# Kernel tuning notes

Measured on AMD Instinct MI355X. Metric: run time of the kernel, lower is better.

Reference implementation:

```python
import jax, jax.numpy as jnp
import numpy as np

B, S = 4096, 4096
NS, FDIM = 16, 64


def _ln(x, g, b):
    mu = jnp.mean(x, axis=-1, keepdims=True)
    v = jnp.mean((x - mu) ** 2, axis=-1, keepdims=True)
    return (x - mu) / jnp.sqrt(v + 1e-5) * g + b


def _rolling_vol_mean(returns, w):
    # mean over all length-w windows of unbiased std (matches per-window torch.std loop)
    Bn, L = returns.shape
    z = jnp.zeros((Bn, 1), returns.dtype)
    c1 = jnp.concatenate([z, jnp.cumsum(returns, axis=1)], axis=1)
    c2 = jnp.concatenate([z, jnp.cumsum(returns * returns, axis=1)], axis=1)
    s = c1[:, w:] - c1[:, :-w]    # [B, L-w+1] window sums
    s2 = c2[:, w:] - c2[:, :-w]
    var = (s2 - s * s / w) / (w - 1)
    return jnp.mean(jnp.sqrt(jnp.maximum(var, 0.0)), axis=1, keepdims=True)


def setup_inputs() -> dict:
    key = jax.random.key(0)
    ks = jax.random.split(key, 24)
    r = lambda i, shp: jax.random.normal(ks[i], shp, jnp.float32) * 0.05
    return {
        'price_series': jax.random.uniform(ks[0], (B, S, 1), jnp.float32) * 10.0 + 1.0,
        're_W': r(1, (4, 4, 64)), 're_b': r(2, (4, 64)),
        're_g': jnp.ones((4, 64), jnp.float32), 're_beta': jnp.zeros((4, 64), jnp.float32),
        'rh_W1': r(3, (256, 64)), 'rh_b1': r(4, (64,)), 'rh_W2': r(5, (64, 4)), 'rh_b2': r(6, (4,)),
        'rv_W': r(7, (3, 128)), 'rv_b': r(8, (128,)),
        'rv_g': jnp.ones((128,), jnp.float32), 'rv_beta': jnp.zeros((128,), jnp.float32),
        'vs_W': r(9, (128, 128)), 'vs_b': r(10, (128,)),
        'vs_g': jnp.ones((128,), jnp.float32), 'vs_beta': jnp.zeros((128,), jnp.float32),
        'vc_W1': r(11, (256, 64)), 'vc_b1': r(12, (64,)), 'vc_W2': r(13, (64, 4)), 'vc_b2': r(14, (4,)),
        'emb': r(15, (NS, FDIM)),
        'cn_W1': r(16, (576, 128)), 'cn_b1': r(17, (128,)),
        'cn_W2': r(18, (128, 64)), 'cn_b2': r(19, (64,)),
        'cn_W3': r(20, (64, 1)), 'cn_b3': r(21, (1,)),
    }


def reference(price_series, re_W, re_b, re_g, re_beta, rh_W1, rh_b1, rh_W2, rh_b2,
              rv_W, rv_b, rv_g, rv_beta, vs_W, vs_b, vs_g, vs_beta,
              vc_W1, vc_b1, vc_W2, vc_b2, emb, cn_W1, cn_b1, cn_W2, cn_b2, cn_W3, cn_b3):
    prices = price_series[:, :, 0]            # [B,S]
    Bn, Sn = prices.shape
    # --- MarketRegimeEncoder: SMA-20 via prefix sums (the per-step torch loop) ---
    cs = jnp.cumsum(prices, axis=1)
    shifted = jnp.concatenate([jnp.zeros((Bn, 20), prices.dtype), cs[:, :-20]], axis=1)
    counts = jnp.minimum(jnp.arange(Sn) + 1, 20).astype(prices.dtype)
    sma20 = (cs - shifted) / counts           # (sma_5 is computed but unused in original)
    trend = jnp.mean((prices - sma20) / (sma20 + 1e-8), axis=1, keepdims=True)
    p10 = prices[:, Sn - 10:Sn - 9]
    momentum = (prices[:, -1:] - p10) / (p10 + 1e-8)
    pmean = jnp.mean(prices, axis=1, keepdims=True)
    mean_rev = (prices[:, -1:] - pmean) / (pmean + 1e-8)
    pstd = jnp.std(prices, axis=1, keepdims=True, ddof=1)
    cycle = pstd / (pmean + 1e-8)
    combined = jnp.concatenate([trend, momentum, mean_rev, cycle], axis=1)  # [B,4]
    h = jax.nn.relu(jnp.einsum('bi,kio->bko', combined, re_W) + re_b[None])  # [B,4,64]
    h = _ln(h, re_g[None], re_beta[None])
    regime_features = h.reshape(Bn, -1)        # [B,256] (trend|momentum|mean_rev|cycle)
    logits = jax.nn.relu(regime_features @ rh_W1 + rh_b1) @ rh_W2 + rh_b2
    regime_probs = jax.nn.softmax(logits, axis=1)
    # --- VolatilityEncodingModule ---
    logp = jnp.log(jnp.maximum(price_series, 1e-8))
    returns = jnp.diff(logp, axis=1)[:, :, 0]  # [B,S-1]
    vol_in = jnp.concatenate([_rolling_vol_mean(returns, w) for w in (5, 10, 20)], axis=1)  # [B,3]
    rv = _ln(jax.nn.relu(vol_in @ rv_W + rv_b), rv_g, rv_beta)
    vs = _ln(jax.nn.relu(rv @ vs_W + vs_b), vs_g, vs_beta)
    vol_features = jnp.concatenate([rv, vs], axis=1)  # [B,256]
    vlogits = jax.nn.relu(vol_features @ vc_W1 + vc_b1) @ vc_W2 + vc_b2
    vol_regime = jax.nn.softmax(vlogits, axis=1)
    # --- OptionsStrategyEncoder: vectorized over strategies ---
    mv = jnp.concatenate([regime_features, vol_features], axis=1)  # [B,512]
    mvp = mv @ cn_W1[:512]                    # [B,128]
    ep = emb @ cn_W1[512:]                    # [NS,128]
    h1 = jax.nn.relu(mvp[:, None, :] + ep[None, :, :] + cn_b1)  # [B,NS,128]
    h2 = jax.nn.relu(h1 @ cn_W2 + cn_b2)      # [B,NS,64]
    scores = (h2 @ cn_W3 + cn_b3)[:, :, 0]    # [B,NS]
    return regime_features, regime_probs, vol_features, vol_regime, scores
```

## Files before the change

### kernel.cpp

```cpp
#include <hip/hip_runtime.h>
#include <math.h>

#define NROWS 4096
#define SLEN  4096
#define RETN  4095
#define STRD  274

__global__ __launch_bounds__(256) void k_ep(const float* __restrict__ emb,
                                            const float* __restrict__ cn_W1,
                                            const float* __restrict__ cn_b1,
                                            float* __restrict__ ep) {
    int idx = blockIdx.x * 256 + threadIdx.x;
    if (idx >= 16 * 128) return;
    int n = idx >> 7, o = idx & 127;
    float acc = cn_b1[o];
    const float* w = cn_W1 + 512 * 128;
    for (int i = 0; i < 64; ++i) acc = fmaf(emb[n * 64 + i], w[i * 128 + o], acc);
    ep[idx] = acc;
}

__global__ __launch_bounds__(256, 4) void k_stats(const float* __restrict__ price,
                                                  float* __restrict__ combined,
                                                  float* __restrict__ volin) {
    __shared__ float scm[16 * STRD];
    __shared__ float red[6][4];

    const int tid = threadIdx.x;
    const int row = blockIdx.x;
    const float* pr = price + (size_t)row * SLEN;

    float pA = 0.f, pB = 0.f;
    if (tid == 0) { pA = pr[SLEN - 10]; pB = pr[SLEN - 1]; }

    if (tid < 32) scm[(tid & 15) * STRD + (tid >> 4)] = 0.f;
    scm[(tid & 15) * STRD + 258 + (tid >> 4)] = 0.f;

    #pragma unroll
    for (int it = 0; it < 4; ++it) {
        const int i = it * 256 + tid;
        const float4 v = ((const float4*)pr)[i];
        const int base = (4 * (i & 3)) * STRD + (i >> 2) + 2;
        scm[base]            = v.x;
        scm[base + STRD]     = v.y;
        scm[base + 2 * STRD] = v.z;
        scm[base + 3 * STRD] = v.w;
    }
    __syncthreads();

    const int s0 = tid * 16;

    float hb[20];
    #pragma unroll
    for (int k = 0; k < 20; ++k)
        hb[k] = (k < 4) ? scm[(12 + k) * STRD + tid]
                        : scm[(k - 4) * STRD + (tid + 1)];
    float x_[16];
    #pragma unroll
    for (int d = 0; d < 16; ++d) x_[d] = scm[d * STRD + (tid + 2)];

    float W = 0.f;
    #pragma unroll
    for (int k = 0; k < 20; ++k) W += hb[k];
    float st = 0.f, s1p = 0.f, s2p = 0.f;
    #pragma unroll
    for (int d = 0; d < 16; ++d) {
        const float x = x_[d];
        W += x - hb[d];
        float inv_cnt = 0.05f;
        if (s0 == 0)                 inv_cnt = 1.0f / (float)(d + 1);
        else if (s0 == 16 && d < 3)  inv_cnt = 1.0f / (float)(17 + d);
        const float sma = W * inv_cnt;
        st  = fmaf(x - sma, __builtin_amdgcn_rcpf(sma + 1e-8f), st);
        s1p += x;
        s2p = fmaf(x, x, s2p);
    }

    float lg[17];
    #pragma unroll
    for (int d = 0; d < 16; ++d) lg[d] = __builtin_amdgcn_logf(fmaxf(x_[d], 1e-8f));
    lg[16] = __builtin_amdgcn_logf(fmaxf(scm[0 * STRD + (tid + 3)], 1e-8f));
    float rs[20];
    #pragma unroll
    for (int d = 0; d < 16; ++d) rs[d] = lg[d + 1] - lg[d];

    __syncthreads();

    #pragma unroll
    for (int d = 0; d < 16; ++d)
        if (s0 + d < RETN) scm[d * STRD + (tid + 2)] = rs[d];
    __syncthreads();

    #pragma unroll
    for (int j = 0; j < 4; ++j) rs[16 + j] = scm[j * STRD + (tid + 3)];

    float S5 = 0.f, Q5 = 0.f, S10 = 0.f, Q10 = 0.f, S20 = 0.f, Q20 = 0.f;
    #pragma unroll
    for (int j = 0; j < 20; ++j) {
        const float x = rs[j];
        S20 += x; Q20 = fmaf(x, x, Q20);
        if (j < 10) { S10 += x; Q10 = fmaf(x, x, Q10); }
        if (j < 5)  { S5  += x; Q5  = fmaf(x, x, Q5); }
    }

    #define SQT(S, Q, invw, invw1) \
        __builtin_amdgcn_sqrtf(fmaxf(fmaf(-(S) * (invw), (S), (Q)) * (invw1), 0.f))
    #define X5(d)  ((d) < 15 ? rs[(d) + 5]  : scm[4 * STRD + (tid + 3)])
    #define X10(d) ((d) < 10 ? rs[(d) + 10] : scm[((d) - 6) * STRD + (tid + 3)])
    #define X20(d) ((d) < 12 ? scm[((d) + 4) * STRD + (tid + 3)] \
                             : scm[((d) - 12) * STRD + (tid + 4)])

    float v5 = 0.f, v10 = 0.f, v20 = 0.f;
    if (tid < 254) {
        #pragma unroll
        for (int d = 0; d < 16; ++d) {
            v5  += SQT(S5,  Q5,  0.2f,  0.25f);
            v10 += SQT(S10, Q10, 0.1f,  1.f / 9.f);
            v20 += SQT(S20, Q20, 0.05f, 1.f / 19.f);
            const float xo = rs[d], qo = xo * xo;
            const float a5 = X5(d), a10 = X10(d), a20 = X20(d);
            S5  += a5  - xo;  Q5  = fmaf(a5,  a5,  Q5)  - qo;
            S10 += a10 - xo;  Q10 = fmaf(a10, a10, Q10) - qo;
            S20 += a20 - xo;  Q20 = fmaf(a20, a20, Q20) - qo;
        }
    } else {
        #pragma unroll
        for (int d = 0; d < 16; ++d) {
            const int i = s0 + d;
            if (i < 4091) v5  += SQT(S5,  Q5,  0.2f,  0.25f);
            if (i < 4086) v10 += SQT(S10, Q10, 0.1f,  1.f / 9.f);
            if (i < 4076) v20 += SQT(S20, Q20, 0.05f, 1.f / 19.f);
            const float xo = rs[d], qo = xo * xo;
            const float a5 = X5(d), a10 = X10(d), a20 = X20(d);
            S5  += a5  - xo;  Q5  = fmaf(a5,  a5,  Q5)  - qo;
            S10 += a10 - xo;  Q10 = fmaf(a10, a10, Q10) - qo;
            S20 += a20 - xo;  Q20 = fmaf(a20, a20, Q20) - qo;
        }
    }
    #undef SQT
    #undef X5
    #undef X10
    #undef X20

    {
        float vals[6] = {s1p, s2p, st, v5, v10, v20};
        const int lane = tid & 63, wid = tid >> 6;
        #pragma unroll
        for (int v = 0; v < 6; ++v) {
            float x = vals[v];
            for (int o = 32; o > 0; o >>= 1) x += __shfl_xor(x, o, 64);
            if (lane == 0) red[v][wid] = x;
        }
    }
    __syncthreads();
    if (tid == 0) {
        const float sum_p  = red[0][0] + red[0][1] + red[0][2] + red[0][3];
        const float sum_p2 = red[1][0] + red[1][1] + red[1][2] + red[1][3];
        const float sum_t  = red[2][0] + red[2][1] + red[2][2] + red[2][3];
        const float sv5    = red[3][0] + red[3][1] + red[3][2] + red[3][3];
        const float sv10   = red[4][0] + red[4][1] + red[4][2] + red[4][3];
        const float sv20   = red[5][0] + red[5][1] + red[5][2] + red[5][3];
        const float pmean = sum_p * (1.f / 4096.f);
        const float varp  = fmaf(-sum_p * (1.f / 4096.f), sum_p, sum_p2) * (1.f / 4095.f);
        const float pstd  = __builtin_amdgcn_sqrtf(fmaxf(varp, 0.f));
        const float ipm   = __builtin_amdgcn_rcpf(pmean + 1e-8f);
        combined[row * 4 + 0] = sum_t * (1.f / 4096.f);
        combined[row * 4 + 1] = (pB - pA) * __builtin_amdgcn_rcpf(pA + 1e-8f);
        combined[row * 4 + 2] = (pB - pmean) * ipm;
        combined[row * 4 + 3] = pstd * ipm;
        const float LN2 = 0.6931471805599453f;
        volin[row * 3 + 0] = sv5  * (LN2 / 4091.f);
        volin[row * 3 + 1] = sv10 * (LN2 / 4086.f);
        volin[row * 3 + 2] = sv20 * (LN2 / 4076.f);
    }
}

__global__ __launch_bounds__(256) void k_mlp(const float* __restrict__ combined,
                                             const float* __restrict__ volin,
                                             const float* __restrict__ re_W,  const float* __restrict__ re_b,
                                             const float* __restrict__ re_g,  const float* __restrict__ re_be,
                                             const float* __restrict__ rh_W1, const float* __restrict__ rh_b1,
                                             const float* __restrict__ rh_W2, const float* __restrict__ rh_b2,
                                             const float* __restrict__ rv_W,  const float* __restrict__ rv_b,
                                             const float* __restrict__ rv_g,  const float* __restrict__ rv_be,
                                             const float* __restrict__ vs_W,  const float* __restrict__ vs_b,
                                             const float* __restrict__ vs_g,  const float* __restrict__ vs_be,
                                             const float* __restrict__ vc_W1, const float* __restrict__ vc_b1,
                                             const float* __restrict__ vc_W2, const float* __restrict__ vc_b2,
                                             float* __restrict__ out_rf, float* __restrict__ out_rp,
                                             float* __restrict__ out_vf, float* __restrict__ out_vr) {
    __shared__ float rf_lds[8][256];
    __shared__ float vf_lds[8][256];
    __shared__ float ps[4][8][64];
    __shared__ float hid_s[8][64];
    __shared__ float prt[4][8];
    __shared__ float cmb_s[8][4];
    __shared__ float vol_s[8][3];

    const int tid  = threadIdx.x;
    const int lane = tid & 63;
    const int wid  = tid >> 6;
    const int row0 = blockIdx.x * 8;

    if (tid < 32) cmb_s[tid >> 2][tid & 3] = combined[(size_t)(row0 + (tid >> 2)) * 4 + (tid & 3)];
    else if (tid < 56) { int t = tid - 32; vol_s[t / 3][t % 3] = volin[(size_t)(row0 + t / 3) * 3 + t % 3]; }
    __syncthreads();

    {
        const float* w = re_W + wid * 256;
        const float w0 = w[lane], w1 = w[64 + lane], w2 = w[128 + lane], w3 = w[192 + lane];
        const float b  = re_b[wid * 64 + lane];
        const float gg = re_g[wid * 64 + lane], bb = re_be[wid * 64 + lane];
        float h[8], sm[8], sq[8];
        #pragma unroll
        for (int r = 0; r < 8; ++r) {
            float v = fmaf(cmb_s[r][0], w0, fmaf(cmb_s[r][1], w1,
                      fmaf(cmb_s[r][2], w2, fmaf(cmb_s[r][3], w3, b))));
            h[r] = fmaxf(v, 0.f);
            sm[r] = h[r]; sq[r] = h[r] * h[r];
        }
        #pragma unroll
        for (int off = 32; off > 0; off >>= 1) {
            #pragma unroll
            for (int r = 0; r < 8; ++r) {
                sm[r] += __shfl_xor(sm[r], off, 64);
                sq[r] += __shfl_xor(sq[r], off, 64);
            }
        }
        #pragma unroll
        for (int r = 0; r < 8; ++r) {
            const float mu  = sm[r] * (1.f / 64.f);
            const float var = fmaxf(sq[r] * (1.f / 64.f) - mu * mu, 0.f);
            const float y = (h[r] - mu) * rsqrtf(var + 1e-5f) * gg + bb;
            rf_lds[r][wid * 64 + lane] = y;
            out_rf[(size_t)(row0 + r) * 256 + wid * 64 + lane] = y;
        }
    }
    __syncthreads();

    {
        const int i0 = wid * 64;
        float acc[8] = {0.f, 0.f, 0.f, 0.f, 0.f, 0.f, 0.f, 0.f};
        for (int i = 0; i < 64; ++i) {
            const float wv = rh_W1[(size_t)(i0 + i) * 64 + lane];
            #pragma unroll
            for (int r = 0; r < 8; ++r) acc[r] = fmaf(rf_lds[r][i0 + i], wv, acc[r]);
        }
        #pragma unroll
        for (int r = 0; r < 8; ++r) ps[wid][r][lane] = acc[r];
    }
    __syncthreads();

    for (int it = tid; it < 512; it += 256) {
        const int r = it >> 6, o = it & 63;
        const float v = ps[0][r][o] + ps[1][r][o] + ps[2][r][o] + ps[3][r][o] + rh_b1[o];
        hid_s[r][o] = fmaxf(v, 0.f);
    }
    __syncthreads();

    if (tid < 32) {
        const int r = tid >> 2, j = tid & 3;
        float acc = rh_b2[j];
        for (int i = 0; i < 64; ++i) acc = fmaf(hid_s[r][i], rh_W2[i * 4 + j], acc);
        float m = acc;
        m = fmaxf(m, __shfl_xor(m, 1, 64));
        m = fmaxf(m, __shfl_xor(m, 2, 64));
        const float e = expf(acc - m);
        float s = e;
        s += __shfl_xor(s, 1, 64);
        s += __shfl_xor(s, 2, 64);
        out_rp[(size_t)(row0 + r) * 4 + j] = e / s;
    }

    {
        const int o = tid & 127, g = tid >> 7, wv_ = tid >> 6;
        const float w0 = rv_W[o], w1 = rv_W[128 + o], w2 = rv_W[256 + o];
        const float b = rv_b[o], gg = rv_g[o], bb = rv_be[o];
        float h[4], sm[4], sq[4];
        #pragma unroll
        for (int r4 = 0; r4 < 4; ++r4) {
            const int r = g * 4 + r4;
            float v = fmaf(vol_s[r][0], w0, fmaf(vol_s[r][1], w1, fmaf(vol_s[r][2], w2, b)));
            h[r4] = fmaxf(v, 0.f);
            sm[r4] = h[r4]; sq[r4] = h[r4] * h[r4];
        }
        #pragma unroll
        for (int off = 32; off > 0; off >>= 1) {
            #pragma unroll
            for (int r4 = 0; r4 < 4; ++r4) {
                sm[r4] += __shfl_xor(sm[r4], off, 64);
                sq[r4] += __shfl_xor(sq[r4], off, 64);
            }
        }
        if (lane == 0) {
            #pragma unroll
            for (int r4 = 0; r4 < 4; ++r4) { prt[wv_][r4 * 2] = sm[r4]; prt[wv_][r4 * 2 + 1] = sq[r4]; }
        }
        __syncthreads();
        #pragma unroll
        for (int r4 = 0; r4 < 4; ++r4) {
            const float S = prt[2 * g][2 * r4]     + prt[2 * g + 1][2 * r4];
            const float Q = prt[2 * g][2 * r4 + 1] + prt[2 * g + 1][2 * r4 + 1];
            const float mu  = S * (1.f / 128.f);
            const float var = fmaxf(Q * (1.f / 128.f) - mu * mu, 0.f);
            const float y = (h[r4] - mu) * rsqrtf(var + 1e-5f) * gg + bb;
            vf_lds[g * 4 + r4][o] = y;
            out_vf[(size_t)(row0 + g * 4 + r4) * 256 + o] = y;
        }
    }
    __syncthreads();

    {
        const int o = tid & 127, g = tid >> 7, wv_ = tid >> 6;
        float acc[4];
        const float b = vs_b[o];
        #pragma unroll
        for (int r4 = 0; r4 < 4; ++r4) acc[r4] = b;
        for (int i = 0; i < 128; ++i) {
            const float wv = vs_W[(size_t)i * 128 + o];
            #pragma unroll
            for (int r4 = 0; r4 < 4; ++r4) acc[r4] = fmaf(vf_lds[g * 4 + r4][i], wv, acc[r4]);
        }
        const float gg = vs_g[o], bb = vs_be[o];
        float h[4], sm[4], sq[4];
        #pragma unroll
        for (int r4 = 0; r4 < 4; ++r4) {
            h[r4] = fmaxf(acc[r4], 0.f);
            sm[r4] = h[r4]; sq[r4] = h[r4] * h[r4];
        }
        #pragma unroll
        for (int off = 32; off > 0; off >>= 1) {
            #pragma unroll
            for (int r4 = 0; r4 < 4; ++r4) {
                sm[r4] += __shfl_xor(sm[r4], off, 64);
                sq[r4] += __shfl_xor(sq[r4], off, 64);
            }
        }
        __syncthreads();
        if (lane == 0) {
            #pragma unroll
            for (int r4 = 0; r4 < 4; ++r4) { prt[wv_][r4 * 2] = sm[r4]; prt[wv_][r4 * 2 + 1] = sq[r4]; }
        }
        __syncthreads();
        #pragma unroll
        for (int r4 = 0; r4 < 4; ++r4) {
            const float S = prt[2 * g][2 * r4]     + prt[2 * g + 1][2 * r4];
            const float Q = prt[2 * g][2 * r4 + 1] + prt[2 * g + 1][2 * r4 + 1];
            const float mu  = S * (1.f / 128.f);
            const float var = fmaxf(Q * (1.f / 128.f) - mu * mu, 0.f);
            const float y = (h[r4] - mu) * rsqrtf(var + 1e-5f) * gg + bb;
            vf_lds[g * 4 + r4][128 + o] = y;
            out_vf[(size_t)(row0 + g * 4 + r4) * 256 + 128 + o] = y;
        }
    }
    __syncthreads();

    {
        const int i0 = wid * 64;
        float acc[8] = {0.f, 0.f, 0.f, 0.f, 0.f, 0.f, 0.f, 0.f};
        for (int i = 0; i < 64; ++i) {
            const float wv = vc_W1[(size_t)(i0 + i) * 64 + lane];
            #pragma unroll
            for (int r = 0; r < 8; ++r) acc[r] = fmaf(vf_lds[r][i0 + i], wv, acc[r]);
        }
        #pragma unroll
        for (int r = 0; r < 8; ++r) ps[wid][r][lane] = acc[r];
    }
    __syncthreads();

    for (int it = tid; it < 512; it += 256) {
        const int r = it >> 6, o = it & 63;
        const float v = ps[0][r][o] + ps[1][r][o] + ps[2][r][o] + ps[3][r][o] + vc_b1[o];
        hid_s[r][o] = fmaxf(v, 0.f);
    }
    __syncthreads();
    if (tid < 32) {
        const int r = tid >> 2, j = tid & 3;
        float acc = vc_b2[j];
        for (int i = 0; i < 64; ++i) acc = fmaf(hid_s[r][i], vc_W2[i * 4 + j], acc);
        float m = acc;
        m = fmaxf(m, __shfl_xor(m, 1, 64));
        m = fmaxf(m, __shfl_xor(m, 2, 64));
        const float e = expf(acc - m);
        float s = e;
        s += __shfl_xor(s, 1, 64);
        s += __shfl_xor(s, 2, 64);
        out_vr[(size_t)(row0 + r) * 4 + j] = e / s;
    }
}

__global__ __launch_bounds__(256, 4) void k_cross(const float* __restrict__ rfin,
                                                  const float* __restrict__ vfin,
                                                  const float* __restrict__ cn_W1,
                                                  const float* __restrict__ cn_W2,
                                                  const float* __restrict__ cn_b2,
                                                  const float* __restrict__ cn_W3,
                                                  const float* __restrict__ cn_b3,
                                                  const float* __restrict__ ep,
                                                  float* __restrict__ scores) {
    __shared__ __align__(16) float ps[4][4][128];
    __shared__ __align__(16) float mvp_s[4][128];
    __shared__ __align__(16) float epb[16][132];

    const int tid  = threadIdx.x;
    const int lane = tid & 63;
    const int wv   = tid >> 6;
    const int row0 = blockIdx.x * 4;

    const float4 ep0 = ((const float4*)ep)[tid];
    const float4 ep1 = ((const float4*)ep)[tid + 256];

    {
        const float* mvbase = (wv < 2)
            ? (rfin + (size_t)row0 * 256 + wv * 128)
            : (vfin + (size_t)row0 * 256 + (wv - 2) * 128);
        float acc0[4] = {0.f, 0.f, 0.f, 0.f};
        float acc1[4] = {0.f, 0.f, 0.f, 0.f};
        for (int ib = 0; ib < 128; ib += 4) {
            float4 m4[4];
            #pragma unroll
            for (int r = 0; r < 4; ++r) m4[r] = *(const float4*)(mvbase + r * 256 + ib);
            const float* w1p = cn_W1 + (size_t)(wv * 128 + ib) * 128 + lane;
            {   const float wa = w1p[0],   wb = w1p[64];
                #pragma unroll
                for (int r = 0; r < 4; ++r) { acc0[r] = fmaf(m4[r].x, wa, acc0[r]); acc1[r] = fmaf(m4[r].x, wb, acc1[r]); } }
            {   const float wa = w1p[128], wb = w1p[192];
                #pragma unroll
                for (int r = 0; r < 4; ++r) { acc0[r] = fmaf(m4[r].y, wa, acc0[r]); acc1[r] = fmaf(m4[r].y, wb, acc1[r]); } }
            {   const float wa = w1p[256], wb = w1p[320];
                #pragma unroll
                for (int r = 0; r < 4; ++r) { acc0[r] = fmaf(m4[r].z, wa, acc0[r]); acc1[r] = fmaf(m4[r].z, wb, acc1[r]); } }
            {   const float wa = w1p[384], wb = w1p[448];
                #pragma unroll
                for (int r = 0; r < 4; ++r) { acc0[r] = fmaf(m4[r].w, wa, acc0[r]); acc1[r] = fmaf(m4[r].w, wb, acc1[r]); } }
        }
        #pragma unroll
        for (int r = 0; r < 4; ++r) {
            ps[wv][r][lane]      = acc0[r];
            ps[wv][r][64 + lane] = acc1[r];
        }
    }
    *(float4*)&epb[tid >> 5][(tid & 31) * 4]       = ep0;
    *(float4*)&epb[8 + (tid >> 5)][(tid & 31) * 4] = ep1;
    __syncthreads();

    #pragma unroll
    for (int k = 0; k < 2; ++k) {
        const int idx = k * 256 + tid;
        const int r = idx >> 7, c = idx & 127;
        mvp_s[r][c] = ps[0][r][c] + ps[1][r][c] + ps[2][r][c] + ps[3][r][c];
    }
    __syncthreads();

    {
        const int ns = tid >> 4;
        const int t  = tid & 15;
        const float* W2c = cn_W2 + 4 * t;
        float acc[4][4];
        #pragma unroll
        for (int r = 0; r < 4; ++r)
            #pragma unroll
            for (int k = 0; k < 4; ++k) acc[r][k] = 0.f;

        for (int cb = 0; cb < 128; cb += 4) {
            float4 m4[4];
            #pragma unroll
            for (int r = 0; r < 4; ++r) m4[r] = *(const float4*)&mvp_s[r][cb];
            const float4 e4 = *(const float4*)&epb[ns][cb];
            {   const float4 w2v = *(const float4*)(W2c + (size_t)(cb + 0) * 64);
                #pragma unroll
                for (int r = 0; r < 4; ++r) {
                    const float h = fmaxf(m4[r].x + e4.x, 0.f);
                    acc[r][0] = fmaf(h, w2v.x, acc[r][0]); acc[r][1] = fmaf(h, w2v.y, acc[r][1]);
                    acc[r][2] = fmaf(h, w2v.z, acc[r][2]); acc[r][3] = fmaf(h, w2v.w, acc[r][3]); } }
            {   const float4 w2v = *(const float4*)(W2c + (size_t)(cb + 1) * 64);
                #pragma unroll
                for (int r = 0; r < 4; ++r) {
                    const float h = fmaxf(m4[r].y + e4.y, 0.f);
                    acc[r][0] = fmaf(h, w2v.x, acc[r][0]); acc[r][1] = fmaf(h, w2v.y, acc[r][1]);
                    acc[r][2] = fmaf(h, w2v.z, acc[r][2]); acc[r][3] = fmaf(h, w2v.w, acc[r][3]); } }
            {   const float4 w2v = *(const float4*)(W2c + (size_t)(cb + 2) * 64);
                #pragma unroll
                for (int r = 0; r < 4; ++r) {
                    const float h = fmaxf(m4[r].z + e4.z, 0.f);
                    acc[r][0] = fmaf(h, w2v.x, acc[r][0]); acc[r][1] = fmaf(h, w2v.y, acc[r][1]);
                    acc[r][2] = fmaf(h, w2v.z, acc[r][2]); acc[r][3] = fmaf(h, w2v.w, acc[r][3]); } }
            {   const float4 w2v = *(const float4*)(W2c + (size_t)(cb + 3) * 64);
                #pragma unroll
                for (int r = 0; r < 4; ++r) {
                    const float h = fmaxf(m4[r].w + e4.w, 0.f);
                    acc[r][0] = fmaf(h, w2v.x, acc[r][0]); acc[r][1] = fmaf(h, w2v.y, acc[r][1]);
                    acc[r][2] = fmaf(h, w2v.z, acc[r][2]); acc[r][3] = fmaf(h, w2v.w, acc[r][3]); } }
        }

        const float4 b2v = *(const float4*)(cn_b2 + 4 * t);
        const float4 w3v = *(const float4*)(cn_W3 + 4 * t);
        const float  b3v = cn_b3[0];
        float sres[4];
        #pragma unroll
        for (int r = 0; r < 4; ++r) {
            float s =      fmaxf(acc[r][0] + b2v.x, 0.f) * w3v.x;
            s = fmaf(fmaxf(acc[r][1] + b2v.y, 0.f), w3v.y, s);
            s = fmaf(fmaxf(acc[r][2] + b2v.z, 0.f), w3v.z, s);
            s = fmaf(fmaxf(acc[r][3] + b2v.w, 0.f), w3v.w, s);
            s += __shfl_xor(s, 1, 64);
            s += __shfl_xor(s, 2, 64);
            s += __shfl_xor(s, 4, 64);
            s += __shfl_xor(s, 8, 64);
            sres[r] = s + b3v;
        }
        if (t == 0) {
            #pragma unroll
            for (int r = 0; r < 4; ++r)
                scores[(size_t)(row0 + r) * 16 + ns] = sres[r];
        }
    }
}

extern "C" void kernel_launch(void* const* d_in, const int* in_sizes, int n_in,
                              void* d_out, int out_size, void* d_ws, size_t ws_size,
                              hipStream_t stream) {
    (void)in_sizes; (void)n_in; (void)out_size; (void)ws_size;

    const float* price = (const float*)d_in[0];
    const float* re_W  = (const float*)d_in[1];
    const float* re_b  = (const float*)d_in[2];
    const float* re_g  = (const float*)d_in[3];
    const float* re_be = (const float*)d_in[4];
    const float* rh_W1 = (const float*)d_in[5];
    const float* rh_b1 = (const float*)d_in[6];
    const float* rh_W2 = (const float*)d_in[7];
    const float* rh_b2 = (const float*)d_in[8];
    const float* rv_W  = (const float*)d_in[9];
    const float* rv_b  = (const float*)d_in[10];
    const float* rv_g  = (const float*)d_in[11];
    const float* rv_be = (const float*)d_in[12];
    const float* vs_W  = (const float*)d_in[13];
    const float* vs_b  = (const float*)d_in[14];
    const float* vs_g  = (const float*)d_in[15];
    const float* vs_be = (const float*)d_in[16];
    const float* vc_W1 = (const float*)d_in[17];
    const float* vc_b1 = (const float*)d_in[18];
    const float* vc_W2 = (const float*)d_in[19];
    const float* vc_b2 = (const float*)d_in[20];
    const float* emb   = (const float*)d_in[21];
    const float* cn_W1 = (const float*)d_in[22];
    const float* cn_b1 = (const float*)d_in[23];
    const float* cn_W2 = (const float*)d_in[24];
    const float* cn_b2 = (const float*)d_in[25];
    const float* cn_W3 = (const float*)d_in[26];
    const float* cn_b3 = (const float*)d_in[27];

    float* out    = (float*)d_out;
    float* out_rf = out;
    float* out_rp = out_rf + 4096 * 256;
    float* out_vf = out_rp + 4096 * 4;
    float* out_vr = out_vf + 4096 * 256;
    float* out_sc = out_vr + 4096 * 4;

    float* ws       = (float*)d_ws;
    float* combined = ws;
    float* volin    = combined + 4096 * 4;
    float* ep       = volin + 4096 * 3;

    hipLaunchKernelGGL(k_ep,    dim3(8),    dim3(256), 0, stream, emb, cn_W1, cn_b1, ep);
    hipLaunchKernelGGL(k_stats, dim3(4096), dim3(256), 0, stream, price, combined, volin);
    hipLaunchKernelGGL(k_mlp,   dim3(512),  dim3(256), 0, stream, combined, volin,
                       re_W, re_b, re_g, re_be, rh_W1, rh_b1, rh_W2, rh_b2,
                       rv_W, rv_b, rv_g, rv_be, vs_W, vs_b, vs_g, vs_be,
                       vc_W1, vc_b1, vc_W2, vc_b2,
                       out_rf, out_rp, out_vf, out_vr);
    hipLaunchKernelGGL(k_cross, dim3(1024), dim3(256), 0, stream, out_rf, out_vf,
                       cn_W1, cn_W2, cn_b2, cn_W3, cn_b3, ep, out_sc);
}
```

Before: 110.1 us.

## Double k_cross threads with split-K reductions across eight waves

k_cross now runs 512 threads per block instead of 256. The first GEMV's K dimension is split across 8 waves instead of 4, and the second layer's 128-wide reduction is split into two halves whose partials are combined through shared memory. The aim is more latency hiding and shorter per-thread serial loops in a kernel with only 1024 blocks. The cost is an extra barrier plus shared-memory reduction, and a larger shared footprint (16KB uni buffer), which may limit resident blocks.

After: 120.9 us. 1.1x slower.

```diff
diff --git a/kernel.cpp b/kernel.cpp
--- a/kernel.cpp
+++ b/kernel.cpp
@@ -388,7 +388,7 @@
     }
 }
 
-__global__ __launch_bounds__(256, 4) void k_cross(const float* __restrict__ rfin,
+__global__ __launch_bounds__(512, 8) void k_cross(const float* __restrict__ rfin,
                                                   const float* __restrict__ vfin,
                                                   const float* __restrict__ cn_W1,
                                                   const float* __restrict__ cn_W2,
@@ -397,7 +397,7 @@
                                                   const float* __restrict__ cn_b3,
                                                   const float* __restrict__ ep,
                                                   float* __restrict__ scores) {
-    __shared__ __align__(16) float ps[4][4][128];
+    __shared__ __align__(16) float uni[4096];
     __shared__ __align__(16) float mvp_s[4][128];
     __shared__ __align__(16) float epb[16][132];
 
@@ -406,20 +406,17 @@
     const int wv   = tid >> 6;
     const int row0 = blockIdx.x * 4;
 
-    const float4 ep0 = ((const float4*)ep)[tid];
-    const float4 ep1 = ((const float4*)ep)[tid + 256];
-
-    {
-        const float* mvbase = (wv < 2)
-            ? (rfin + (size_t)row0 * 256 + wv * 128)
-            : (vfin + (size_t)row0 * 256 + (wv - 2) * 128);
+    {
+        const float* mvbase = (wv < 4)
+            ? (rfin + (size_t)row0 * 256 + wv * 64)
+            : (vfin + (size_t)row0 * 256 + (wv - 4) * 64);
         float acc0[4] = {0.f, 0.f, 0.f, 0.f};
         float acc1[4] = {0.f, 0.f, 0.f, 0.f};
-        for (int ib = 0; ib < 128; ib += 4) {
+        for (int ib = 0; ib < 64; ib += 4) {
             float4 m4[4];
             #pragma unroll
             for (int r = 0; r < 4; ++r) m4[r] = *(const float4*)(mvbase + r * 256 + ib);
-            const float* w1p = cn_W1 + (size_t)(wv * 128 + ib) * 128 + lane;
+            const float* w1p = cn_W1 + (size_t)(wv * 64 + ib) * 128 + lane;
             {   const float wa = w1p[0],   wb = w1p[64];
                 #pragma unroll
                 for (int r = 0; r < 4; ++r) { acc0[r] = fmaf(m4[r].x, wa, acc0[r]); acc1[r] = fmaf(m4[r].x, wb, acc1[r]); } }
@@ -435,67 +432,86 @@
         }
         #pragma unroll
         for (int r = 0; r < 4; ++r) {
-            ps[wv][r][lane]      = acc0[r];
-            ps[wv][r][64 + lane] = acc1[r];
-        }
-    }
-    *(float4*)&epb[tid >> 5][(tid & 31) * 4]       = ep0;
-    *(float4*)&epb[8 + (tid >> 5)][(tid & 31) * 4] = ep1;
-    __syncthreads();
-
-    #pragma unroll
-    for (int k = 0; k < 2; ++k) {
-        const int idx = k * 256 + tid;
-        const int r = idx >> 7, c = idx & 127;
-        mvp_s[r][c] = ps[0][r][c] + ps[1][r][c] + ps[2][r][c] + ps[3][r][c];
-    }
-    __syncthreads();
-
-    {
-        const int ns = tid >> 4;
-        const int t  = tid & 15;
+            uni[wv * 512 + r * 128 + lane]      = acc0[r];
+            uni[wv * 512 + r * 128 + 64 + lane] = acc1[r];
+        }
+    }
+    {
+        const int ns = tid >> 5, c4 = (tid & 31) * 4;
+        *(float4*)&epb[ns][c4] = *(const float4*)(ep + ns * 128 + c4);
+    }
+    __syncthreads();
+
+    {
+        const int r = tid >> 7, c = tid & 127;
+        float s = 0.f;
+        #pragma unroll
+        for (int w = 0; w < 8; ++w) s += uni[w * 512 + r * 128 + c];
+        mvp_s[r][c] = s;
+    }
+    __syncthreads();
+
+    const int ch  = tid >> 8;
+    const int nst = tid & 255;
+    const int ns  = nst >> 4;
+    const int t   = nst & 15;
+    float acc[4][4];
+    #pragma unroll
+    for (int r = 0; r < 4; ++r)
+        #pragma unroll
+        for (int k = 0; k < 4; ++k) acc[r][k] = 0.f;
+    {
+        const int c0 = ch * 64;
         const float* W2c = cn_W2 + 4 * t;
-        float acc[4][4];
-        #pragma unroll
-        for (int r = 0; r < 4; ++r)
-            #pragma unroll
-            for (int k = 0; k < 4; ++k) acc[r][k] = 0.f;
-
-        for (int cb = 0; cb < 128; cb += 4) {
+        #pragma unroll 2
+        for (int cb = 0; cb < 64; cb += 4) {
+            const int c = c0 + cb;
             float4 m4[4];
             #pragma unroll
-            for (int r = 0; r < 4; ++r) m4[r] = *(const float4*)&mvp_s[r][cb];
-            const float4 e4 = *(const float4*)&epb[ns][cb];
-            {   const float4 w2v = *(const float4*)(W2c + (size_t)(cb + 0) * 64);
+            for (int r = 0; r < 4; ++r) m4[r] = *(const float4*)&mvp_s[r][c];
+            const float4 e4 = *(const float4*)&epb[ns][c];
+            {   const float4 w2v = *(const float4*)(W2c + (size_t)(c + 0) * 64);
                 #pragma unroll
                 for (int r = 0; r < 4; ++r) {
                     const float h = fmaxf(m4[r].x + e4.x, 0.f);
                     acc[r][0] = fmaf(h, w2v.x, acc[r][0]); acc[r][1] = fmaf(h, w2v.y, acc[r][1]);
                     acc[r][2] = fmaf(h, w2v.z, acc[r][2]); acc[r][3] = fmaf(h, w2v.w, acc[r][3]); } }
-            {   const float4 w2v = *(const float4*)(W2c + (size_t)(cb + 1) * 64);
+            {   const float4 w2v = *(const float4*)(W2c + (size_t)(c + 1) * 64);
                 #pragma unroll
                 for (int r = 0; r < 4; ++r) {
                     const float h = fmaxf(m4[r].y + e4.y, 0.f);
                     acc[r][0] = fmaf(h, w2v.x, acc[r][0]); acc[r][1] = fmaf(h, w2v.y, acc[r][1]);
                     acc[r][2] = fmaf(h, w2v.z, acc[r][2]); acc[r][3] = fmaf(h, w2v.w, acc[r][3]); } }
-            {   const float4 w2v = *(const float4*)(W2c + (size_t)(cb + 2) * 64);
+            {   const float4 w2v = *(const float4*)(W2c + (size_t)(c + 2) * 64);
                 #pragma unroll
                 for (int r = 0; r < 4; ++r) {
                     const float h = fmaxf(m4[r].z + e4.z, 0.f);
                     acc[r][0] = fmaf(h, w2v.x, acc[r][0]); acc[r][1] = fmaf(h, w2v.y, acc[r][1]);
                     acc[r][2] = fmaf(h, w2v.z, acc[r][2]); acc[r][3] = fmaf(h, w2v.w, acc[r][3]); } }
-            {   const float4 w2v = *(const float4*)(W2c + (size_t)(cb + 3) * 64);
+            {   const float4 w2v = *(const float4*)(W2c + (size_t)(c + 3) * 64);
                 #pragma unroll
                 for (int r = 0; r < 4; ++r) {
                     const float h = fmaxf(m4[r].w + e4.w, 0.f);
                     acc[r][0] = fmaf(h, w2v.x, acc[r][0]); acc[r][1] = fmaf(h, w2v.y, acc[r][1]);
                     acc[r][2] = fmaf(h, w2v.z, acc[r][2]); acc[r][3] = fmaf(h, w2v.w, acc[r][3]); } }
         }
-
+    }
+    __syncthreads();
+    if (ch == 1) {
+        #pragma unroll
+        for (int r = 0; r < 4; ++r)
+            *(float4*)&uni[nst * 16 + r * 4] = make_float4(acc[r][0], acc[r][1], acc[r][2], acc[r][3]);
+    }
+    __syncthreads();
+    if (ch == 0) {
+        #pragma unroll
+        for (int r = 0; r < 4; ++r) {
+            const float4 o = *(const float4*)&uni[nst * 16 + r * 4];
+            acc[r][0] += o.x; acc[r][1] += o.y; acc[r][2] += o.z; acc[r][3] += o.w;
+        }
         const float4 b2v = *(const float4*)(cn_b2 + 4 * t);
         const float4 w3v = *(const float4*)(cn_W3 + 4 * t);
         const float  b3v = cn_b3[0];
-        float sres[4];
         #pragma unroll
         for (int r = 0; r < 4; ++r) {
             float s =      fmaxf(acc[r][0] + b2v.x, 0.f) * w3v.x;
@@ -506,12 +522,7 @@
             s += __shfl_xor(s, 2, 64);
             s += __shfl_xor(s, 4, 64);
             s += __shfl_xor(s, 8, 64);
-            sres[r] = s + b3v;
-        }
-        if (t == 0) {
-            #pragma unroll
-            for (int r = 0; r < 4; ++r)
-                scores[(size_t)(row0 + r) * 16 + ns] = sres[r];
+            if (t == 0) scores[(size_t)(row0 + r) * 16 + ns] = s + b3v;
         }
     }
 }
@@ -569,6 +580,6 @@
                        rv_W, rv_b, rv_g, rv_be, vs_W, vs_b, vs_g, vs_be,
                        vc_W1, vc_b1, vc_W2, vc_b2,
                        out_rf, out_rp, out_vf, out_vr);
-    hipLaunchKernelGGL(k_cross, dim3(1024), dim3(256), 0, stream, out_rf, out_vf,
+    hipLaunchKernelGGL(k_cross, dim3(1024), dim3(512), 0, stream, out_rf, out_vf,
                        cn_W1, cn_W2, cn_b2, cn_W3, cn_b3, ep, out_sc);
 }
```
